# Kernel optimization log

Hardware: AMD Instinct MI355X
Metric: run time of the kernel (lower is better)

The kernel has to match this reference:

```python
import jax, jax.numpy as jnp
import numpy as np

D = 256          # embed_dim
NH = 4           # num_heads
NE = 16          # num_hyperedges
TC = 512         # text_channels
WIN = 64         # window size
EPS = 1e-5


def setup_inputs() -> dict:
    key = jax.random.key(0)
    ks = jax.random.split(key, 20)
    s = 0.02
    return {
        "feature_map": jax.random.normal(ks[0], (8, 256, 64, 64), jnp.float32),
        "text_features": jax.random.normal(ks[1], (8, 64, TC), jnp.float32),
        # qkv_gen: Conv2d(256->256,1x1), GELU, Conv2d(256->768,3x3,pad1), GroupNorm(4,768)
        "conv1_w": jax.random.normal(ks[2], (D, 256, 1, 1), jnp.float32) * s,
        "conv1_b": jnp.zeros((D,), jnp.float32),
        "conv2_w": jax.random.normal(ks[3], (3 * D, D, 3, 3), jnp.float32) * s,
        "conv2_b": jnp.zeros((3 * D,), jnp.float32),
        "gn_w": jnp.ones((3 * D,), jnp.float32),
        "gn_b": jnp.zeros((3 * D,), jnp.float32),
        # shared nn.MultiheadAttention params
        "in_proj_w": jax.random.normal(ks[4], (3 * D, D), jnp.float32) * s,
        "in_proj_b": jnp.zeros((3 * D,), jnp.float32),
        "out_proj_w": jax.random.normal(ks[5], (D, D), jnp.float32) * s,
        "out_proj_b": jnp.zeros((D,), jnp.float32),
        # text_adapter Linear(512->256)
        "txt_w": jax.random.normal(ks[6], (D, TC), jnp.float32) * s,
        "txt_b": jnp.zeros((D,), jnp.float32),
        # edge_predictor: Linear(512->256), GELU, Linear(256->16)
        "ep1_w": jax.random.normal(ks[7], (D, 2 * D), jnp.float32) * s,
        "ep1_b": jnp.zeros((D,), jnp.float32),
        "ep2_w": jax.random.normal(ks[8], (NE, D), jnp.float32) * s,
        "ep2_b": jnp.zeros((NE,), jnp.float32),
    }


def _gelu(x):
    return jax.nn.gelu(x, approximate=False)  # torch default is exact erf GELU


def _conv(x, w, b, pad):
    y = jax.lax.conv_general_dilated(x, w, (1, 1), [(pad, pad), (pad, pad)],
                                     dimension_numbers=("NCHW", "OIHW", "NCHW"))
    return y + b[None, :, None, None]


def _group_norm(x, w, b, groups=4):
    B, C, H, W = x.shape
    xg = x.reshape(B, groups, C // groups, H, W)
    mu = xg.mean(axis=(2, 3, 4), keepdims=True)
    var = xg.var(axis=(2, 3, 4), keepdims=True)
    xg = (xg - mu) * jax.lax.rsqrt(var + EPS)
    return xg.reshape(B, C, H, W) * w[None, :, None, None] + b[None, :, None, None]


def _mha(q, k, v, in_w, in_b, out_w, out_b):
    # torch nn.MultiheadAttention (batch_first), same-dim q/k/v
    Wq, Wk, Wv = in_w[:D], in_w[D:2 * D], in_w[2 * D:]
    bq, bk, bv = in_b[:D], in_b[D:2 * D], in_b[2 * D:]
    dh = D // NH

    def split(x, W, bias):
        y = x @ W.T + bias                      # [B,L,D]
        Bv, L, _ = y.shape
        return y.reshape(Bv, L, NH, dh).transpose(0, 2, 1, 3)  # [B,H,L,dh]

    qh, kh, vh = split(q, Wq, bq), split(k, Wk, bk), split(v, Wv, bv)
    scores = jnp.einsum("bhqd,bhkd->bhqk", qh, kh) / jnp.sqrt(jnp.float32(dh))
    attn = jax.nn.softmax(scores, axis=-1)
    o = jnp.einsum("bhqk,bhkd->bhqd", attn, vh)
    Bv, _, Lq, _ = o.shape
    o = o.transpose(0, 2, 1, 3).reshape(Bv, Lq, D)
    return o @ out_w.T + out_b


def reference(feature_map, text_features, conv1_w, conv1_b, conv2_w, conv2_b,
              gn_w, gn_b, in_proj_w, in_proj_b, out_proj_w, out_proj_b,
              txt_w, txt_b, ep1_w, ep1_b, ep2_w, ep2_b):
    B, C, H, W = feature_map.shape
    N = H * W
    # qkv_gen
    x = _gelu(_conv(feature_map, conv1_w, conv1_b, 0))
    qkv = _group_norm(_conv(x, conv2_w, conv2_b, 1), gn_w, gn_b)
    q, k, v = jnp.split(qkv, 3, axis=1)                    # each [B,D,H,W]
    to_seq = lambda t: t.reshape(B, D, N).transpose(0, 2, 1)  # [B,N,D]
    q_seq, k_seq, v_seq = to_seq(q), to_seq(k), to_seq(v)

    # text_adapter: Linear then AdaptiveAvgPool1d(4) over sequence (L=64 -> 4 bins of 16)
    t = text_features @ txt_w.T + txt_b                    # [B,L,D]
    L = t.shape[1]
    text_feat = t.reshape(B, 4, L // 4, D).mean(axis=2)    # [B,4,D]

    # hierarchical attention
    nw = N // WIN
    q_win = q_seq.reshape(B * nw, WIN, D)
    k_win = k_seq.reshape(B * nw, WIN, D)
    v_win = v_seq.reshape(B * nw, WIN, D)
    local = _mha(q_win, k_win, v_win, in_proj_w, in_proj_b, out_proj_w, out_proj_b)
    local = local.reshape(B, nw, WIN, D)
    global_q = local.mean(axis=2)                          # [B,nw,D]
    glob = _mha(global_q, text_feat, text_feat, in_proj_w, in_proj_b, out_proj_w, out_proj_b)
    glob = jnp.broadcast_to(glob[:, :, None, :], (B, nw, WIN, D))

    combined = jnp.concatenate([local.reshape(B, N, D), glob.reshape(B, N, D)], axis=-1)
    h = _gelu(combined @ ep1_w.T + ep1_b)
    return jax.nn.sigmoid(h @ ep2_w.T + ep2_b)             # [B,N,16]
```

## Files before the change

kernel.cpp:

```cpp
#include <hip/hip_runtime.h>

#define DEV __device__ __forceinline__

typedef __attribute__((ext_vector_type(8))) short bfx8;
typedef __attribute__((ext_vector_type(4))) float fx4;

typedef __attribute__((address_space(3))) unsigned int as3_u32;
typedef const __attribute__((address_space(1))) unsigned int as1_u32c;

DEV void gl_lds16(const void* g, const void* l) {
  __builtin_amdgcn_global_load_lds((as1_u32c*)(unsigned long long)g,
                                   (as3_u32*)(unsigned long long)l, 16, 0, 0);
}

DEV short f2bf(float f) {
  unsigned u = __float_as_uint(f);
  u += 0x7fffu + ((u >> 16) & 1u);
  return (short)(u >> 16);
}
DEV float bf2f(short s) {
  return __uint_as_float(((unsigned)(unsigned short)s) << 16);
}
DEV float gelu_f(float x) { return 0.5f * x * (1.0f + erff(x * 0.70710678118654752f)); }

#define MFMA16(acc, a, b) (acc) = __builtin_amdgcn_mfma_f32_16x16x32_bf16((a), (b), (acc), 0, 0, 0)

struct CvtSeg { const float* src; short* dst; int n; };
struct CvtArgs { CvtSeg s[7]; };

__global__ __launch_bounds__(256) void cvt_multi(CvtArgs a) {
  CvtSeg s = a.s[blockIdx.y];
  int i = ((int)blockIdx.x * 256 + (int)threadIdx.x) * 8;
  if (i >= s.n) return;
  bfx8 o;
  #pragma unroll
  for (int j = 0; j < 8; ++j) o[j] = f2bf(s.src[i + j]);
  *(bfx8*)(s.dst + i) = o;
}

__global__ __launch_bounds__(256) void cvt_conv2w(const float* src, short* dst) {
  int oc = (int)blockIdx.x * 256 + (int)threadIdx.x;
  const float* s = src + (long)oc * 9;
  float t[9];
  #pragma unroll
  for (int j = 0; j < 9; ++j) t[j] = s[j];
  #pragma unroll
  for (int tap = 0; tap < 9; ++tap)
    dst[(long)tap * (768 * 256) + oc] = f2bf(t[tap]);
}

__global__ __launch_bounds__(256) void transpose_wo(const float* ow, short* WoT) {
  __shared__ float tile[64][65];
  int c0 = blockIdx.x * 64, d0 = blockIdx.y * 64;
  int tp = threadIdx.x & 63, tr = threadIdx.x >> 6;
  #pragma unroll
  for (int i = 0; i < 16; ++i) {
    int c = tr + i * 4;
    tile[c][tp] = ow[(long)(c0 + c) * 256 + d0 + tp];
  }
  __syncthreads();
  #pragma unroll
  for (int i = 0; i < 16; ++i) {
    int d = tr + i * 4;
    WoT[(long)(d0 + d) * 256 + c0 + tp] = f2bf(tile[tp][d]);
  }
}

__global__ __launch_bounds__(64) void ebc2(const float* e1w, const float* e1b, const float* ob, float* ebc) {
  int n = blockIdx.x, lane = threadIdx.x;
  float s = 0.0f;
  #pragma unroll
  for (int i = 0; i < 4; ++i) {
    int c = lane + 64 * i;
    s += ob[c] * e1w[(long)n * 512 + c];
  }
  #pragma unroll
  for (int off = 1; off < 64; off <<= 1) s += __shfl_xor(s, off);
  if (lane == 0) ebc[n] = e1b[n] + s;
}

DEV int axc(int p, int c) { return p * 260 + (c ^ (((p >> 2) & 7) << 2)); }

__global__ __launch_bounds__(256) void tc1(const float* fm, const short* W1bf,
                                           const float* b1, short* xP) {
  __shared__ float Af[64 * 260];
  const int lane = threadIdx.x & 63, wv = threadIdx.x >> 6;
  const int lg = lane >> 4, li = lane & 15;
  const int y = blockIdx.x & 63, b = blockIdx.x >> 6;
  const float* src = fm + (long)b * 256 * 4096 + y * 64;
  #pragma unroll
  for (int i = 0; i < 16; ++i) {
    int chunk = i * 256 + (int)threadIdx.x;
    int c = chunk >> 4;
    int q = chunk & 15;
    fx4 v = *(const fx4*)(src + (long)c * 4096 + q * 4);
    #pragma unroll
    for (int j = 0; j < 4; ++j) Af[axc(q * 4 + j, c)] = v[j];
  }
  __syncthreads();

  fx4 acc[4][4] = {};
  const short* Bb = W1bf + (long)(wv * 64 + li) * 256 + lg * 8;
  for (int c0 = 0; c0 < 256; c0 += 32) {
    bfx8 af[4], bfr[4];
    #pragma unroll
    for (int mi = 0; mi < 4; ++mi) {
      int p = mi * 16 + li;
      fx4 lo = *(const fx4*)(&Af[axc(p, c0 + lg * 8)]);
      fx4 hi = *(const fx4*)(&Af[axc(p, c0 + lg * 8 + 4)]);
      bfx8 t;
      t[0] = f2bf(lo[0]); t[1] = f2bf(lo[1]); t[2] = f2bf(lo[2]); t[3] = f2bf(lo[3]);
      t[4] = f2bf(hi[0]); t[5] = f2bf(hi[1]); t[6] = f2bf(hi[2]); t[7] = f2bf(hi[3]);
      af[mi] = t;
    }
    #pragma unroll
    for (int ni = 0; ni < 4; ++ni) bfr[ni] = *(const bfx8*)(Bb + ni * 16 * 256 + c0);
    #pragma unroll
    for (int mi = 0; mi < 4; ++mi)
      #pragma unroll
      for (int ni = 0; ni < 4; ++ni) MFMA16(acc[mi][ni], af[mi], bfr[ni]);
  }

  short* dstP = xP + ((long)b * 66 * 66 + (long)(y + 1) * 66 + 1) * 256;
  #pragma unroll
  for (int mi = 0; mi < 4; ++mi)
    #pragma unroll
    for (int ni = 0; ni < 4; ++ni) {
      int col = wv * 64 + ni * 16 + li;
      float bias = b1[col];
      #pragma unroll
      for (int r = 0; r < 4; ++r) {
        int x = mi * 16 + 4 * lg + r;
        dstP[(long)x * 256 + col] = f2bf(gelu_f(acc[mi][ni][r] + bias));
      }
    }
}

struct GemmP {
  const short* A; const short* B; void* O;
  const float* biasN; const float* biasM; const float* rowbias;
  long lda, ldb, ldo, sA, sB, sO;
  int M, N, K, outF32, act, padHW;
  int aShift;
  long sBN, sBM;
};

__global__ __launch_bounds__(256) void gemm128(GemmP g) {
  __shared__ short As[128 * 32];
  __shared__ short Bs[128 * 32];
  const int lane = threadIdx.x & 63, wv = threadIdx.x >> 6;
  const int wm = wv >> 1, wn = wv & 1;
  const int lg = lane >> 4, li = lane & 15;
  const int m0 = blockIdx.y * 128, n0 = blockIdx.x * 128, z = blockIdx.z;
  const short* A = g.A + (long)z * g.sA + (long)(n0 >> 8) * g.aShift;
  const short* B = g.B + (long)z * g.sB;
  const int srow = wv * 16 + (lane >> 2);
  const int scol = (lane & 3) * 8;
  const short* pA0 = A + (long)(m0 + srow) * g.lda + scol;
  const short* pA1 = A + (long)(m0 + 64 + srow) * g.lda + scol;
  const short* pB0 = B + (long)(n0 + srow) * g.ldb + scol;
  const short* pB1 = B + (long)(n0 + 64 + srow) * g.ldb + scol;
  short* ldsA = As + wv * 512;
  short* ldsB = Bs + wv * 512;
  const short* aRd = As + (wm * 64 + li) * 32 + lg * 8;
  const short* bRd = Bs + (wn * 64 + li) * 32 + lg * 8;

  fx4 acc[4][4] = {};
  for (int kc = 0; kc < g.K; kc += 32) {
    gl_lds16(pA0 + kc, ldsA);
    gl_lds16(pA1 + kc, ldsA + 2048);
    gl_lds16(pB0 + kc, ldsB);
    gl_lds16(pB1 + kc, ldsB + 2048);
    __syncthreads();
    bfx8 af[4], bf[4];
    #pragma unroll
    for (int mi = 0; mi < 4; ++mi) af[mi] = *(const bfx8*)(aRd + mi * 16 * 32);
    #pragma unroll
    for (int ni = 0; ni < 4; ++ni) bf[ni] = *(const bfx8*)(bRd + ni * 16 * 32);
    #pragma unroll
    for (int mi = 0; mi < 4; ++mi)
      #pragma unroll
      for (int ni = 0; ni < 4; ++ni)
        MFMA16(acc[mi][ni], af[mi], bf[ni]);
    __syncthreads();
  }

  #pragma unroll
  for (int mi = 0; mi < 4; ++mi)
    #pragma unroll
    for (int ni = 0; ni < 4; ++ni) {
      int col = n0 + wn * 64 + ni * 16 + li;
      int rowb = m0 + wm * 64 + mi * 16 + 4 * lg;
      float bn = g.biasN ? g.biasN[(long)z * g.sBN + col] : 0.0f;
      #pragma unroll
      for (int r = 0; r < 4; ++r) {
        int row = rowb + r;
        float v = acc[mi][ni][r] + bn;
        if (g.biasM) v += g.biasM[(long)z * g.sBM + row];
        if (g.rowbias) v += g.rowbias[(long)(row >> 6) * g.N + col];
        if (g.act == 1) v = gelu_f(v);
        long orow = row;
        if (g.padHW) orow = (long)((row >> 6) + 1) * 66 + (row & 63) + 1;
        long oidx = (long)z * g.sO + orow * g.ldo + col;
        if (g.outF32) ((float*)g.O)[oidx] = v;
        else ((short*)g.O)[oidx] = f2bf(v);
      }
    }
}

__global__ __launch_bounds__(256) void conv2g(const short* xP, const short* W2t,
                                              const float* b2, short* qkv, float* stats) {
  __shared__ short As[2 * 128 * 32];
  __shared__ short Bs[2 * 128 * 32];
  __shared__ float red[4][4];
  const int lane = threadIdx.x & 63, wv = threadIdx.x >> 6;
  const int wm = wv >> 1, wn = wv & 1;
  const int lg = lane >> 4, li = lane & 15;
  const int w = ((int)blockIdx.x & 7) * 192 + ((int)blockIdx.x >> 3);
  const int n0 = (w % 6) * 128;
  const int by = w / 6;
  const int b = by >> 5, ypair = by & 31;
  const short* xPb = xP + (long)b * 66 * 66 * 256;

  const int srow = wv * 16 + (lane >> 2);
  const int scol = (lane & 3) * 8;
  long baseA[2], baseB[2];
  #pragma unroll
  for (int j = 0; j < 2; ++j) {
    int r = j * 64 + srow;
    int yy = 2 * ypair + (r >> 6);
    int x = r & 63;
    baseA[j] = ((long)yy * 66 + x) * 256 + scol;
    baseB[j] = (long)(n0 + r) * 256 + scol;
  }
  short* ldsA = As + wv * 512;
  short* ldsB = Bs + wv * 512;
  const short* aRd = As + (wm * 64 + li) * 32 + lg * 8;
  const short* bRd = Bs + (wn * 64 + li) * 32 + lg * 8;

  fx4 acc[4][4] = {};
  for (int ks = 0; ks < 36; ++ks) {
    int tap = ks >> 2;
    int c0 = (ks & 3) * 64;
    int dy = tap / 3, dx = tap - dy * 3;
    long aoff = (long)(dy * 66 + dx) * 256 + c0;
    long boff = (long)tap * (768 * 256) + c0;
    gl_lds16(xPb + baseA[0] + aoff, ldsA);
    gl_lds16(xPb + baseA[1] + aoff, ldsA + 2048);
    gl_lds16(xPb + baseA[0] + aoff + 32, ldsA + 4096);
    gl_lds16(xPb + baseA[1] + aoff + 32, ldsA + 6144);
    gl_lds16(W2t + baseB[0] + boff, ldsB);
    gl_lds16(W2t + baseB[1] + boff, ldsB + 2048);
    gl_lds16(W2t + baseB[0] + boff + 32, ldsB + 4096);
    gl_lds16(W2t + baseB[1] + boff + 32, ldsB + 6144);
    __syncthreads();
    #pragma unroll
    for (int kk = 0; kk < 2; ++kk) {
      bfx8 af[4], bf[4];
      #pragma unroll
      for (int mi = 0; mi < 4; ++mi) af[mi] = *(const bfx8*)(aRd + kk * 4096 + mi * 16 * 32);
      #pragma unroll
      for (int ni = 0; ni < 4; ++ni) bf[ni] = *(const bfx8*)(bRd + kk * 4096 + ni * 16 * 32);
      #pragma unroll
      for (int mi = 0; mi < 4; ++mi)
        #pragma unroll
        for (int ni = 0; ni < 4; ++ni)
          MFMA16(acc[mi][ni], af[mi], bf[ni]);
    }
    __syncthreads();
  }

  const int g0 = n0 / 192;
  const int bnd = (g0 + 1) * 192;
  float sA = 0.0f, s2A = 0.0f, sB = 0.0f, s2B = 0.0f;
  const long prow0 = (long)b * 4096 + (long)ypair * 128 + wm * 64 + 4 * lg;
  #pragma unroll
  for (int ni = 0; ni < 4; ++ni) {
    int col = n0 + wn * 64 + ni * 16 + li;
    float bias = b2[col];
    bool inA = (col < bnd);
    #pragma unroll
    for (int mi = 0; mi < 4; ++mi) {
      long rb = prow0 + mi * 16;
      #pragma unroll
      for (int r = 0; r < 4; ++r) {
        float v = acc[mi][ni][r] + bias;
        if (inA) { sA += v; s2A += v * v; } else { sB += v; s2B += v * v; }
        qkv[(rb + r) * 768 + col] = f2bf(v);
      }
    }
  }
  #pragma unroll
  for (int off = 1; off < 64; off <<= 1) {
    sA += __shfl_xor(sA, off);  s2A += __shfl_xor(s2A, off);
    sB += __shfl_xor(sB, off);  s2B += __shfl_xor(s2B, off);
  }
  if (lane == 0) { red[wv][0] = sA; red[wv][1] = s2A; red[wv][2] = sB; red[wv][3] = s2B; }
  __syncthreads();
  if (threadIdx.x == 0) {
    float a1 = red[0][0] + red[1][0] + red[2][0] + red[3][0];
    float a2 = red[0][1] + red[1][1] + red[2][1] + red[3][1];
    atomicAdd(&stats[(b * 4 + g0) * 2], a1);
    atomicAdd(&stats[(b * 4 + g0) * 2 + 1], a2);
    if (bnd < n0 + 128) {
      float b1s = red[0][2] + red[1][2] + red[2][2] + red[3][2];
      float b2s = red[0][3] + red[1][3] + red[2][3] + red[3][3];
      atomicAdd(&stats[(b * 4 + g0 + 1) * 2], b1s);
      atomicAdd(&stats[(b * 4 + g0 + 1) * 2 + 1], b2s);
    }
  }
}

__global__ void gn_fin(const float* stats, float* mufs) {
  int i = threadIdx.x;
  if (i >= 32) return;
  float n = 192.0f * 4096.0f;
  float mu = stats[i * 2] / n;
  float var = stats[i * 2 + 1] / n - mu * mu;
  mufs[i * 2] = mu;
  mufs[i * 2 + 1] = rsqrtf(var + 1e-5f);
}

__global__ __launch_bounds__(256) void gn_fold(const float* mufs, const float* gnw, const float* gnb,
                                               const float* inw, const float* inb,
                                               short* Wf, float* bfold) {
  const int lane = threadIdx.x & 63, wv = threadIdx.x >> 6;
  const int row = blockIdx.x * 4 + wv;
  const int b = row / 768, j = row - b * 768;
  const int cb = (j >> 8) << 8;
  float part = 0.0f;
  #pragma unroll
  for (int i = 0; i < 4; ++i) {
    int c = lane + 64 * i;
    int cg = cb + c;
    int grp = cg / 192;
    float mu = mufs[(b * 4 + grp) * 2];
    float rs = mufs[(b * 4 + grp) * 2 + 1];
    float s = rs * gnw[cg];
    float t = gnb[cg] - mu * s;
    float wv_ = inw[(long)j * 256 + c];
    Wf[(long)row * 256 + c] = f2bf(wv_ * s);
    part += t * wv_;
  }
  #pragma unroll
  for (int off = 1; off < 64; off <<= 1) part += __shfl_xor(part, off);
  if (lane == 0) bfold[row] = inb[j] + part;
}

__global__ __launch_bounds__(256) void attn_local(const short* qk, const short* vhT,
                                                  short* oat, short* oatm) {
  __shared__ short Pl[4 * 64 * 72];
  const int lane = threadIdx.x & 63, h = threadIdx.x >> 6;
  const int lg = lane >> 4, li = lane & 15;
  const int bw = blockIdx.x;
  const int b = bw >> 6, wY = bw & 63;
  const long p0 = (long)bw * 64;

  bfx8 qf[4][2], kf[4][2];
  #pragma unroll
  for (int mi = 0; mi < 4; ++mi)
    #pragma unroll
    for (int ks = 0; ks < 2; ++ks) {
      qf[mi][ks] = *(const bfx8*)(qk + (p0 + 16 * mi + li) * 512 + h * 64 + 32 * ks + 8 * lg);
      kf[mi][ks] = *(const bfx8*)(qk + (p0 + 16 * mi + li) * 512 + 256 + h * 64 + 32 * ks + 8 * lg);
    }
  fx4 s[4][4] = {};
  #pragma unroll
  for (int mi = 0; mi < 4; ++mi)
    #pragma unroll
    for (int ni = 0; ni < 4; ++ni) {
      MFMA16(s[mi][ni], qf[mi][0], kf[ni][0]);
      MFMA16(s[mi][ni], qf[mi][1], kf[ni][1]);
    }
  #pragma unroll
  for (int mi = 0; mi < 4; ++mi)
    #pragma unroll
    for (int ni = 0; ni < 4; ++ni) s[mi][ni] *= 0.125f;

  #pragma unroll
  for (int mi = 0; mi < 4; ++mi)
    #pragma unroll
    for (int r = 0; r < 4; ++r) {
      float mx = fmaxf(fmaxf(s[mi][0][r], s[mi][1][r]), fmaxf(s[mi][2][r], s[mi][3][r]));
      for (int off = 1; off < 16; off <<= 1) mx = fmaxf(mx, __shfl_xor(mx, off));
      float e[4];
      float sum = 0.0f;
      #pragma unroll
      for (int ni = 0; ni < 4; ++ni) { e[ni] = expf(s[mi][ni][r] - mx); sum += e[ni]; }
      for (int off = 1; off < 16; off <<= 1) sum += __shfl_xor(sum, off);
      float inv = 1.0f / sum;
      int row = h * 64 + 16 * mi + 4 * lg + r;
      #pragma unroll
      for (int ni = 0; ni < 4; ++ni) Pl[row * 72 + 16 * ni + li] = f2bf(e[ni] * inv);
    }
  __syncthreads();

  fx4 o[4][4] = {};
  #pragma unroll
  for (int ks = 0; ks < 2; ++ks) {
    bfx8 pf[4], vf[4];
    #pragma unroll
    for (int mi = 0; mi < 4; ++mi)
      pf[mi] = *(const bfx8*)(&Pl[(h * 64 + 16 * mi + li) * 72 + 32 * ks + 8 * lg]);
    #pragma unroll
    for (int ni = 0; ni < 4; ++ni)
      vf[ni] = *(const bfx8*)(vhT + ((long)(b * 256 + h * 64 + 16 * ni + li)) * 4096 + wY * 64 + 32 * ks + 8 * lg);
    #pragma unroll
    for (int mi = 0; mi < 4; ++mi)
      #pragma unroll
      for (int ni = 0; ni < 4; ++ni) MFMA16(o[mi][ni], pf[mi], vf[ni]);
  }
  #pragma unroll
  for (int mi = 0; mi < 4; ++mi)
    #pragma unroll
    for (int ni = 0; ni < 4; ++ni)
      #pragma unroll
      for (int r = 0; r < 4; ++r)
        oat[(p0 + 16 * mi + 4 * lg + r) * 256 + h * 64 + 16 * ni + li] = f2bf(o[mi][ni][r]);

  #pragma unroll
  for (int ni = 0; ni < 4; ++ni) {
    float s2 = 0.0f;
    #pragma unroll
    for (int mi = 0; mi < 4; ++mi)
      #pragma unroll
      for (int r = 0; r < 4; ++r) s2 += o[mi][ni][r];
    s2 += __shfl_xor(s2, 16);
    s2 += __shfl_xor(s2, 32);
    if (lg == 0)
      oatm[(long)bw * 256 + h * 64 + 16 * ni + li] = f2bf(s2 * (1.0f / 64.0f));
  }
}

#define GP 272

DEV void mm_stage(const short* srcA, const short* Bw, long ldb, const float* biasN,
                  short* dstL, float* dstG, int wv, int lg, int li) {
  fx4 acc[4][4] = {};
  const short* aRd = srcA + li * GP + lg * 8;
  const short* bR = Bw + (long)(wv * 64 + li) * ldb + lg * 8;
  for (int kc = 0; kc < 256; kc += 32) {
    bfx8 af[4], bf[4];
    #pragma unroll
    for (int mi = 0; mi < 4; ++mi) af[mi] = *(const bfx8*)(aRd + mi * 16 * GP + kc);
    #pragma unroll
    for (int ni = 0; ni < 4; ++ni) bf[ni] = *(const bfx8*)(bR + (long)ni * 16 * ldb + kc);
    #pragma unroll
    for (int mi = 0; mi < 4; ++mi)
      #pragma unroll
      for (int ni = 0; ni < 4; ++ni) MFMA16(acc[mi][ni], af[mi], bf[ni]);
  }
  #pragma unroll
  for (int mi = 0; mi < 4; ++mi)
    #pragma unroll
    for (int ni = 0; ni < 4; ++ni) {
      int col = wv * 64 + ni * 16 + li;
      float bn = biasN[col];
      #pragma unroll
      for (int r = 0; r < 4; ++r) {
        int row = mi * 16 + 4 * lg + r;
        float v = acc[mi][ni][r] + bn;
        if (dstL) dstL[row * GP + col] = f2bf(v);
        else dstG[(long)row * 256 + col] = v;
      }
    }
}

__global__ __launch_bounds__(256) void globk(
    const short* Tbf, const short* oatm,
    const short* Wtxt, const short* Wqkv, const short* Wo, const short* Wep1,
    const float* tb, const float* ob, const float* inb, const float* ebc,
    float* gcon) {
  __shared__ short bufA[64 * GP];
  __shared__ short bufB[64 * GP];
  __shared__ float tmean_s[4][512];
  __shared__ float tfb_s[4][256];
  __shared__ float kh_s[4][256];
  __shared__ float vh_s[4][256];
  const int t = threadIdx.x;
  const int lane = t & 63, wv = t >> 6;
  const int lg = lane >> 4, li = lane & 15;
  const int b = blockIdx.x;

  {
    int key = t >> 6, d0 = (t & 63) * 8;
    float s[8] = {};
    const short* src = Tbf + ((long)(b * 64 + key * 16)) * 512 + d0;
    for (int i = 0; i < 16; ++i) {
      bfx8 v = *(const bfx8*)(src + i * 512);
      #pragma unroll
      for (int j = 0; j < 8; ++j) s[j] += bf2f(v[j]);
    }
    #pragma unroll
    for (int j = 0; j < 8; ++j) tmean_s[key][d0 + j] = s[j] * (1.0f / 16.0f);
  }
  {
    #pragma unroll
    for (int i = 0; i < 8; ++i) {
      int chunk = i * 256 + t;
      int row = chunk >> 5, colc = (chunk & 31) * 8;
      *(bfx8*)(bufA + row * GP + colc) =
          *(const bfx8*)(oatm + ((long)(b * 64 + row)) * 256 + colc);
    }
  }
  __syncthreads();
  {
    int n = t;
    float a0 = 0, a1 = 0, a2 = 0, a3 = 0;
    const short* wr = Wtxt + (long)n * 512;
    for (int d = 0; d < 512; d += 8) {
      bfx8 w = *(const bfx8*)(wr + d);
      #pragma unroll
      for (int j = 0; j < 8; ++j) {
        float wf = bf2f(w[j]);
        a0 += tmean_s[0][d + j] * wf;
        a1 += tmean_s[1][d + j] * wf;
        a2 += tmean_s[2][d + j] * wf;
        a3 += tmean_s[3][d + j] * wf;
      }
    }
    float bias = tb[n];
    tfb_s[0][n] = a0 + bias; tfb_s[1][n] = a1 + bias;
    tfb_s[2][n] = a2 + bias; tfb_s[3][n] = a3 + bias;
  }
  __syncthreads();
  {
    int n = t;
    const short* wk = Wqkv + (long)(256 + n) * 256;
    const short* wvp = Wqkv + (long)(512 + n) * 256;
    float k0=0,k1=0,k2=0,k3=0,v0=0,v1=0,v2=0,v3=0;
    for (int d = 0; d < 256; d += 8) {
      bfx8 wkv = *(const bfx8*)(wk + d);
      bfx8 wvv = *(const bfx8*)(wvp + d);
      #pragma unroll
      for (int j = 0; j < 8; ++j) {
        float f0 = tfb_s[0][d+j], f1 = tfb_s[1][d+j], f2 = tfb_s[2][d+j], f3 = tfb_s[3][d+j];
        float kw = bf2f(wkv[j]), vw = bf2f(wvv[j]);
        k0 += f0*kw; k1 += f1*kw; k2 += f2*kw; k3 += f3*kw;
        v0 += f0*vw; v1 += f1*vw; v2 += f2*vw; v3 += f3*vw;
      }
    }
    float bk = inb[256+n], bv = inb[512+n];
    kh_s[0][n]=k0+bk; kh_s[1][n]=k1+bk; kh_s[2][n]=k2+bk; kh_s[3][n]=k3+bk;
    vh_s[0][n]=v0+bv; vh_s[1][n]=v1+bv; vh_s[2][n]=v2+bv; vh_s[3][n]=v3+bv;
  }
  mm_stage(bufA, Wo, 256, ob, bufB, nullptr, wv, lg, li);
  __syncthreads();
  mm_stage(bufB, Wqkv, 256, inb, bufA, nullptr, wv, lg, li);
  __syncthreads();
  {
    int p = t >> 2, h = t & 3;
    const short* qr = bufA + p * GP + h * 64;
    float sc[4];
    #pragma unroll
    for (int key = 0; key < 4; ++key) {
      float s = 0.0f;
      for (int d = 0; d < 64; d += 8) {
        bfx8 q8 = *(const bfx8*)(qr + d);
        #pragma unroll
        for (int j = 0; j < 8; ++j) s += bf2f(q8[j]) * kh_s[key][h * 64 + d + j];
      }
      sc[key] = s * 0.125f;
    }
    float mx = fmaxf(fmaxf(sc[0], sc[1]), fmaxf(sc[2], sc[3]));
    float e0 = expf(sc[0]-mx), e1 = expf(sc[1]-mx), e2 = expf(sc[2]-mx), e3 = expf(sc[3]-mx);
    float inv = 1.0f / (e0 + e1 + e2 + e3);
    e0 *= inv; e1 *= inv; e2 *= inv; e3 *= inv;
    short* orow = bufB + p * GP + h * 64;
    for (int d = 0; d < 64; ++d) {
      float o = e0*vh_s[0][h*64+d] + e1*vh_s[1][h*64+d] + e2*vh_s[2][h*64+d] + e3*vh_s[3][h*64+d];
      orow[d] = f2bf(o);
    }
  }
  __syncthreads();
  mm_stage(bufB, Wo, 256, ob, bufA, nullptr, wv, lg, li);
  __syncthreads();
  mm_stage(bufA, Wep1 + 256, 512, ebc, nullptr, gcon + (long)b * 64 * 256, wv, lg, li);
}

__global__ __launch_bounds__(256) void ep2k(const short* hb, const short* w2, const float* b2, float* out) {
  int pp = blockIdx.x * 16 + (threadIdx.x >> 4);
  int e = threadIdx.x & 15;
  const short* hr = hb + (long)pp * 256;
  const short* wr = w2 + (long)e * 256;
  float acc = b2[e];
  for (int k = 0; k < 256; k += 8) {
    bfx8 hv = *(const bfx8*)(hr + k);
    bfx8 wv = *(const bfx8*)(wr + k);
    #pragma unroll
    for (int j = 0; j < 8; ++j) acc += bf2f(hv[j]) * bf2f(wv[j]);
  }
  out[(long)pp * 16 + e] = 1.0f / (1.0f + expf(-acc));
}

extern "C" void kernel_launch(void* const* d_in, const int* in_sizes, int n_in,
                              void* d_out, int out_size, void* d_ws, size_t ws_size,
                              hipStream_t stream) {
  (void)in_sizes; (void)n_in; (void)out_size; (void)ws_size;
  const float* fm  = (const float*)d_in[0];
  const float* txt = (const float*)d_in[1];
  const float* w1  = (const float*)d_in[2];
  const float* b1  = (const float*)d_in[3];
  const float* w2  = (const float*)d_in[4];
  const float* b2  = (const float*)d_in[5];
  const float* gnw = (const float*)d_in[6];
  const float* gnb = (const float*)d_in[7];
  const float* inw = (const float*)d_in[8];
  const float* inb = (const float*)d_in[9];
  const float* ow  = (const float*)d_in[10];
  const float* ob  = (const float*)d_in[11];
  const float* tw  = (const float*)d_in[12];
  const float* tb  = (const float*)d_in[13];
  const float* e1w = (const float*)d_in[14];
  const float* e1b = (const float*)d_in[15];
  const float* e2w = (const float*)d_in[16];
  const float* e2b = (const float*)d_in[17];
  float* out = (float*)d_out;

  char* base = (char*)d_ws;
  size_t off = 0;
  auto alloc = [&](size_t bytes) -> char* {
    char* r = base + off;
    off = (off + bytes + 255) & ~(size_t)255;
    return r;
  };
  short* W1bf = (short*)alloc(256 * 256 * 2);
  short* W2t  = (short*)alloc((size_t)9 * 768 * 256 * 2);
  short* Wqkv = (short*)alloc(768 * 256 * 2);
  short* Wo   = (short*)alloc(256 * 256 * 2);
  short* WoT  = (short*)alloc(256 * 256 * 2);
  short* Wcomb= (short*)alloc(256 * 256 * 2);
  float* ebc  = (float*)alloc(256 * 4);
  short* Wtxt = (short*)alloc(256 * 512 * 2);
  short* Wep1 = (short*)alloc(256 * 512 * 2);
  short* Wep2 = (short*)alloc(16 * 256 * 2);
  short* Tbf  = (short*)alloc((size_t)8 * 64 * 512 * 2);
  short* xP   = (short*)alloc((size_t)8 * 66 * 66 * 256 * 2);
  short* qkv  = (short*)alloc((size_t)8 * 4096 * 768 * 2);
  float* stats= (float*)alloc(64 * 4);
  float* mufs = (float*)alloc(64 * 4);
  short* Wf   = (short*)alloc((size_t)8 * 768 * 256 * 2);
  float* bfold= (float*)alloc((size_t)8 * 768 * 4);
  short* qk   = (short*)alloc((size_t)32768 * 512 * 2);
  short* vhT  = (short*)alloc((size_t)8 * 4096 * 256 * 2);
  short* oat  = (short*)alloc((size_t)8 * 4096 * 256 * 2);
  short* oatm = (short*)alloc(512 * 256 * 2);
  float* gcon = (float*)alloc(512 * 256 * 4);
  short* hbuf = (short*)alloc((size_t)8 * 4096 * 256 * 2);

  hipMemsetAsync(stats, 0, 64 * 4, stream);
  hipMemsetAsync(xP, 0, (size_t)8 * 66 * 66 * 256 * 2, stream);

  CvtArgs ca;
  ca.s[0] = {w1,  W1bf, 256 * 256};
  ca.s[1] = {inw, Wqkv, 768 * 256};
  ca.s[2] = {ow,  Wo,   256 * 256};
  ca.s[3] = {tw,  Wtxt, 256 * 512};
  ca.s[4] = {e1w, Wep1, 256 * 512};
  ca.s[5] = {e2w, Wep2, 16 * 256};
  ca.s[6] = {txt, Tbf,  8 * 64 * 512};
  cvt_multi<<<dim3(128, 7), 256, 0, stream>>>(ca);
  cvt_conv2w<<<768, 256, 0, stream>>>(w2, W2t);
  transpose_wo<<<dim3(4, 4), 256, 0, stream>>>(ow, WoT);
  ebc2<<<256, 64, 0, stream>>>(e1w, e1b, ob, ebc);

  {
    GemmP g{};
    g.A = Wep1; g.lda = 512; g.B = WoT; g.ldb = 256;
    g.O = Wcomb; g.ldo = 256;
    g.M = 256; g.N = 256; g.K = 256;
    gemm128<<<dim3(2, 2, 1), 256, 0, stream>>>(g);
  }

  tc1<<<512, 256, 0, stream>>>(fm, W1bf, b1, xP);

  conv2g<<<1536, 256, 0, stream>>>(xP, W2t, b2, qkv, stats);
  gn_fin<<<1, 32, 0, stream>>>(stats, mufs);
  gn_fold<<<1536, 256, 0, stream>>>(mufs, gnw, gnb, inw, inb, Wf, bfold);

  {
    GemmP g{};
    g.A = qkv; g.lda = 768; g.sA = 4096L * 768;
    g.B = Wf; g.ldb = 256; g.sB = 768L * 256;
    g.O = qk; g.ldo = 512; g.sO = 4096L * 512;
    g.biasN = bfold; g.sBN = 768;
    g.aShift = 256;
    g.M = 4096; g.N = 512; g.K = 256;
    gemm128<<<dim3(4, 32, 8), 256, 0, stream>>>(g);
  }
  {
    GemmP g{};
    g.A = Wf + 512 * 256; g.lda = 256; g.sA = 768L * 256;
    g.B = qkv + 512; g.ldb = 768; g.sB = 4096L * 768;
    g.O = vhT; g.ldo = 4096; g.sO = 256L * 4096;
    g.biasM = bfold + 512; g.sBM = 768;
    g.M = 256; g.N = 4096; g.K = 256;
    gemm128<<<dim3(32, 2, 8), 256, 0, stream>>>(g);
  }

  attn_local<<<512, 256, 0, stream>>>(qk, vhT, oat, oatm);

  globk<<<8, 256, 0, stream>>>(Tbf, oatm, Wtxt, Wqkv, Wo, Wep1,
                               tb, ob, inb, ebc, gcon);

  {
    GemmP g{};
    g.A = oat; g.lda = 256; g.B = Wcomb; g.ldb = 256;
    g.O = hbuf; g.ldo = 256; g.rowbias = gcon; g.act = 1;
    g.M = 32768; g.N = 256; g.K = 256;
    gemm128<<<dim3(2, 256, 1), 256, 0, stream>>>(g);
  }

  ep2k<<<2048, 256, 0, stream>>>(hbuf, Wep2, e2b, out);
}
```

Baseline: 392.0 us.

## Fuse local attention, global attention, edge-predictor GEMM and sigmoid head into one kernel

```diff
diff --git a/kernel.cpp b/kernel.cpp
--- a/kernel.cpp
+++ b/kernel.cpp
@@ -347,141 +347,13 @@
   if (lane == 0) bfold[row] = inb[j] + part;
 }
 
-__global__ __launch_bounds__(256) void attn_local(const short* qk, const short* vhT,
-                                                  short* oat, short* oatm) {
-  __shared__ short Pl[4 * 64 * 72];
-  const int lane = threadIdx.x & 63, h = threadIdx.x >> 6;
-  const int lg = lane >> 4, li = lane & 15;
-  const int bw = blockIdx.x;
-  const int b = bw >> 6, wY = bw & 63;
-  const long p0 = (long)bw * 64;
-
-  bfx8 qf[4][2], kf[4][2];
-  #pragma unroll
-  for (int mi = 0; mi < 4; ++mi)
-    #pragma unroll
-    for (int ks = 0; ks < 2; ++ks) {
-      qf[mi][ks] = *(const bfx8*)(qk + (p0 + 16 * mi + li) * 512 + h * 64 + 32 * ks + 8 * lg);
-      kf[mi][ks] = *(const bfx8*)(qk + (p0 + 16 * mi + li) * 512 + 256 + h * 64 + 32 * ks + 8 * lg);
-    }
-  fx4 s[4][4] = {};
-  #pragma unroll
-  for (int mi = 0; mi < 4; ++mi)
-    #pragma unroll
-    for (int ni = 0; ni < 4; ++ni) {
-      MFMA16(s[mi][ni], qf[mi][0], kf[ni][0]);
-      MFMA16(s[mi][ni], qf[mi][1], kf[ni][1]);
-    }
-  #pragma unroll
-  for (int mi = 0; mi < 4; ++mi)
-    #pragma unroll
-    for (int ni = 0; ni < 4; ++ni) s[mi][ni] *= 0.125f;
-
-  #pragma unroll
-  for (int mi = 0; mi < 4; ++mi)
-    #pragma unroll
-    for (int r = 0; r < 4; ++r) {
-      float mx = fmaxf(fmaxf(s[mi][0][r], s[mi][1][r]), fmaxf(s[mi][2][r], s[mi][3][r]));
-      for (int off = 1; off < 16; off <<= 1) mx = fmaxf(mx, __shfl_xor(mx, off));
-      float e[4];
-      float sum = 0.0f;
-      #pragma unroll
-      for (int ni = 0; ni < 4; ++ni) { e[ni] = expf(s[mi][ni][r] - mx); sum += e[ni]; }
-      for (int off = 1; off < 16; off <<= 1) sum += __shfl_xor(sum, off);
-      float inv = 1.0f / sum;
-      int row = h * 64 + 16 * mi + 4 * lg + r;
-      #pragma unroll
-      for (int ni = 0; ni < 4; ++ni) Pl[row * 72 + 16 * ni + li] = f2bf(e[ni] * inv);
-    }
-  __syncthreads();
-
-  fx4 o[4][4] = {};
-  #pragma unroll
-  for (int ks = 0; ks < 2; ++ks) {
-    bfx8 pf[4], vf[4];
-    #pragma unroll
-    for (int mi = 0; mi < 4; ++mi)
-      pf[mi] = *(const bfx8*)(&Pl[(h * 64 + 16 * mi + li) * 72 + 32 * ks + 8 * lg]);
-    #pragma unroll
-    for (int ni = 0; ni < 4; ++ni)
-      vf[ni] = *(const bfx8*)(vhT + ((long)(b * 256 + h * 64 + 16 * ni + li)) * 4096 + wY * 64 + 32 * ks + 8 * lg);
-    #pragma unroll
-    for (int mi = 0; mi < 4; ++mi)
-      #pragma unroll
-      for (int ni = 0; ni < 4; ++ni) MFMA16(o[mi][ni], pf[mi], vf[ni]);
-  }
-  #pragma unroll
-  for (int mi = 0; mi < 4; ++mi)
-    #pragma unroll
-    for (int ni = 0; ni < 4; ++ni)
-      #pragma unroll
-      for (int r = 0; r < 4; ++r)
-        oat[(p0 + 16 * mi + 4 * lg + r) * 256 + h * 64 + 16 * ni + li] = f2bf(o[mi][ni][r]);
-
-  #pragma unroll
-  for (int ni = 0; ni < 4; ++ni) {
-    float s2 = 0.0f;
-    #pragma unroll
-    for (int mi = 0; mi < 4; ++mi)
-      #pragma unroll
-      for (int r = 0; r < 4; ++r) s2 += o[mi][ni][r];
-    s2 += __shfl_xor(s2, 16);
-    s2 += __shfl_xor(s2, 32);
-    if (lg == 0)
-      oatm[(long)bw * 256 + h * 64 + 16 * ni + li] = f2bf(s2 * (1.0f / 64.0f));
-  }
-}
-
-#define GP 272
-
-DEV void mm_stage(const short* srcA, const short* Bw, long ldb, const float* biasN,
-                  short* dstL, float* dstG, int wv, int lg, int li) {
-  fx4 acc[4][4] = {};
-  const short* aRd = srcA + li * GP + lg * 8;
-  const short* bR = Bw + (long)(wv * 64 + li) * ldb + lg * 8;
-  for (int kc = 0; kc < 256; kc += 32) {
-    bfx8 af[4], bf[4];
-    #pragma unroll
-    for (int mi = 0; mi < 4; ++mi) af[mi] = *(const bfx8*)(aRd + mi * 16 * GP + kc);
-    #pragma unroll
-    for (int ni = 0; ni < 4; ++ni) bf[ni] = *(const bfx8*)(bR + (long)ni * 16 * ldb + kc);
-    #pragma unroll
-    for (int mi = 0; mi < 4; ++mi)
-      #pragma unroll
-      for (int ni = 0; ni < 4; ++ni) MFMA16(acc[mi][ni], af[mi], bf[ni]);
-  }
-  #pragma unroll
-  for (int mi = 0; mi < 4; ++mi)
-    #pragma unroll
-    for (int ni = 0; ni < 4; ++ni) {
-      int col = wv * 64 + ni * 16 + li;
-      float bn = biasN[col];
-      #pragma unroll
-      for (int r = 0; r < 4; ++r) {
-        int row = mi * 16 + 4 * lg + r;
-        float v = acc[mi][ni][r] + bn;
-        if (dstL) dstL[row * GP + col] = f2bf(v);
-        else dstG[(long)row * 256 + col] = v;
-      }
-    }
-}
-
-__global__ __launch_bounds__(256) void globk(
-    const short* Tbf, const short* oatm,
-    const short* Wtxt, const short* Wqkv, const short* Wo, const short* Wep1,
-    const float* tb, const float* ob, const float* inb, const float* ebc,
-    float* gcon) {
-  __shared__ short bufA[64 * GP];
-  __shared__ short bufB[64 * GP];
+__global__ __launch_bounds__(256) void globk_txt(const short* Tbf, const short* Wtxt,
+                                                 const short* Wqkv, const float* tb,
+                                                 const float* inb, float* khv, float* vhv) {
   __shared__ float tmean_s[4][512];
   __shared__ float tfb_s[4][256];
-  __shared__ float kh_s[4][256];
-  __shared__ float vh_s[4][256];
   const int t = threadIdx.x;
-  const int lane = t & 63, wv = t >> 6;
-  const int lg = lane >> 4, li = lane & 15;
   const int b = blockIdx.x;
-
   {
     int key = t >> 6, d0 = (t & 63) * 8;
     float s[8] = {};
@@ -493,15 +365,6 @@
     }
     #pragma unroll
     for (int j = 0; j < 8; ++j) tmean_s[key][d0 + j] = s[j] * (1.0f / 16.0f);
-  }
-  {
-    #pragma unroll
-    for (int i = 0; i < 8; ++i) {
-      int chunk = i * 256 + t;
-      int row = chunk >> 5, colc = (chunk & 31) * 8;
-      *(bfx8*)(bufA + row * GP + colc) =
-          *(const bfx8*)(oatm + ((long)(b * 64 + row)) * 256 + colc);
-    }
   }
   __syncthreads();
   {
@@ -541,56 +404,229 @@
       }
     }
     float bk = inb[256+n], bv = inb[512+n];
-    kh_s[0][n]=k0+bk; kh_s[1][n]=k1+bk; kh_s[2][n]=k2+bk; kh_s[3][n]=k3+bk;
-    vh_s[0][n]=v0+bv; vh_s[1][n]=v1+bv; vh_s[2][n]=v2+bv; vh_s[3][n]=v3+bv;
-  }
-  mm_stage(bufA, Wo, 256, ob, bufB, nullptr, wv, lg, li);
-  __syncthreads();
-  mm_stage(bufB, Wqkv, 256, inb, bufA, nullptr, wv, lg, li);
-  __syncthreads();
-  {
-    int p = t >> 2, h = t & 3;
-    const short* qr = bufA + p * GP + h * 64;
-    float sc[4];
-    #pragma unroll
-    for (int key = 0; key < 4; ++key) {
-      float s = 0.0f;
-      for (int d = 0; d < 64; d += 8) {
-        bfx8 q8 = *(const bfx8*)(qr + d);
-        #pragma unroll
-        for (int j = 0; j < 8; ++j) s += bf2f(q8[j]) * kh_s[key][h * 64 + d + j];
+    khv[(b*4+0)*256+n]=k0+bk; khv[(b*4+1)*256+n]=k1+bk;
+    khv[(b*4+2)*256+n]=k2+bk; khv[(b*4+3)*256+n]=k3+bk;
+    vhv[(b*4+0)*256+n]=v0+bv; vhv[(b*4+1)*256+n]=v1+bv;
+    vhv[(b*4+2)*256+n]=v2+bv; vhv[(b*4+3)*256+n]=v3+bv;
+  }
+}
+
+__global__ __launch_bounds__(256) void attn_mega(
+    const short* qk, const short* vhT, const float* khv, const float* vhv,
+    const short* Wo, const short* Wqkv, const short* Wep1, const short* Wcomb, const short* Wep2,
+    const float* ob, const float* inb, const float* ebc, const float* e2b,
+    float* out) {
+  __shared__ short Pl[4 * 64 * 72];
+  __shared__ float vecA[256], vecB[256], vecG[256];
+  __shared__ float scb[16], pb[16];
+  const int t = threadIdx.x;
+  const int lane = t & 63, h = t >> 6;
+  const int lg = lane >> 4, li = lane & 15;
+  const int bw = blockIdx.x;
+  const int b = bw >> 6, wY = bw & 63;
+  const long p0 = (long)bw * 64;
+
+  bfx8 qf[4][2], kf[4][2];
+  #pragma unroll
+  for (int mi = 0; mi < 4; ++mi)
+    #pragma unroll
+    for (int ks = 0; ks < 2; ++ks) {
+      qf[mi][ks] = *(const bfx8*)(qk + (p0 + 16 * mi + li) * 512 + h * 64 + 32 * ks + 8 * lg);
+      kf[mi][ks] = *(const bfx8*)(qk + (p0 + 16 * mi + li) * 512 + 256 + h * 64 + 32 * ks + 8 * lg);
+    }
+  fx4 s[4][4] = {};
+  #pragma unroll
+  for (int mi = 0; mi < 4; ++mi)
+    #pragma unroll
+    for (int ni = 0; ni < 4; ++ni) {
+      MFMA16(s[mi][ni], qf[mi][0], kf[ni][0]);
+      MFMA16(s[mi][ni], qf[mi][1], kf[ni][1]);
+    }
+  #pragma unroll
+  for (int mi = 0; mi < 4; ++mi)
+    #pragma unroll
+    for (int ni = 0; ni < 4; ++ni) s[mi][ni] *= 0.125f;
+
+  #pragma unroll
+  for (int mi = 0; mi < 4; ++mi)
+    #pragma unroll
+    for (int r = 0; r < 4; ++r) {
+      float mx = fmaxf(fmaxf(s[mi][0][r], s[mi][1][r]), fmaxf(s[mi][2][r], s[mi][3][r]));
+      for (int off = 1; off < 16; off <<= 1) mx = fmaxf(mx, __shfl_xor(mx, off));
+      float e[4];
+      float sum = 0.0f;
+      #pragma unroll
+      for (int ni = 0; ni < 4; ++ni) { e[ni] = expf(s[mi][ni][r] - mx); sum += e[ni]; }
+      for (int off = 1; off < 16; off <<= 1) sum += __shfl_xor(sum, off);
+      float inv = 1.0f / sum;
+      int row = h * 64 + 16 * mi + 4 * lg + r;
+      #pragma unroll
+      for (int ni = 0; ni < 4; ++ni) Pl[row * 72 + 16 * ni + li] = f2bf(e[ni] * inv);
+    }
+  __syncthreads();
+
+  fx4 o[4][4] = {};
+  #pragma unroll
+  for (int ks = 0; ks < 2; ++ks) {
+    bfx8 pf[4], vf[4];
+    #pragma unroll
+    for (int mi = 0; mi < 4; ++mi)
+      pf[mi] = *(const bfx8*)(&Pl[(h * 64 + 16 * mi + li) * 72 + 32 * ks + 8 * lg]);
+    #pragma unroll
+    for (int ni = 0; ni < 4; ++ni)
+      vf[ni] = *(const bfx8*)(vhT + ((long)(b * 256 + h * 64 + 16 * ni + li)) * 4096 + wY * 64 + 32 * ks + 8 * lg);
+    #pragma unroll
+    for (int mi = 0; mi < 4; ++mi)
+      #pragma unroll
+      for (int ni = 0; ni < 4; ++ni) MFMA16(o[mi][ni], pf[mi], vf[ni]);
+  }
+
+  #pragma unroll
+  for (int ni = 0; ni < 4; ++ni) {
+    float s2 = 0.0f;
+    #pragma unroll
+    for (int mi = 0; mi < 4; ++mi)
+      #pragma unroll
+      for (int r = 0; r < 4; ++r) s2 += o[mi][ni][r];
+    s2 += __shfl_xor(s2, 16);
+    s2 += __shfl_xor(s2, 32);
+    if (lg == 0) vecA[h * 64 + 16 * ni + li] = s2 * (1.0f / 64.0f);
+  }
+  __syncthreads();
+
+  short* obuf = Pl;
+  #pragma unroll
+  for (int mi = 0; mi < 4; ++mi)
+    #pragma unroll
+    for (int ni = 0; ni < 4; ++ni)
+      #pragma unroll
+      for (int r = 0; r < 4; ++r)
+        obuf[(16 * mi + 4 * lg + r) * 264 + h * 64 + 16 * ni + li] = f2bf(o[mi][ni][r]);
+
+  {
+    float sum = 0.0f;
+    const short* wr = Wo + (long)t * 256;
+    for (int d = 0; d < 256; d += 8) {
+      bfx8 w8 = *(const bfx8*)(wr + d);
+      #pragma unroll
+      for (int j = 0; j < 8; ++j) sum += vecA[d + j] * bf2f(w8[j]);
+    }
+    vecB[t] = sum + ob[t];
+  }
+  __syncthreads();
+  {
+    float sum = 0.0f;
+    const short* wr = Wqkv + (long)t * 256;
+    for (int d = 0; d < 256; d += 8) {
+      bfx8 w8 = *(const bfx8*)(wr + d);
+      #pragma unroll
+      for (int j = 0; j < 8; ++j) sum += vecB[d + j] * bf2f(w8[j]);
+    }
+    vecG[t] = sum + inb[t];
+  }
+  __syncthreads();
+  if (t < 16) {
+    int key = t & 3, hh = t >> 2;
+    float sum = 0.0f;
+    const float* kr = khv + (long)(b * 4 + key) * 256 + hh * 64;
+    for (int d = 0; d < 64; ++d) sum += vecG[hh * 64 + d] * kr[d];
+    scb[hh * 4 + key] = sum * 0.125f;
+  }
+  __syncthreads();
+  if (t < 4) {
+    float s0 = scb[t*4], s1 = scb[t*4+1], s2 = scb[t*4+2], s3 = scb[t*4+3];
+    float mx = fmaxf(fmaxf(s0, s1), fmaxf(s2, s3));
+    float e0 = expf(s0-mx), e1 = expf(s1-mx), e2 = expf(s2-mx), e3 = expf(s3-mx);
+    float inv = 1.0f / (e0 + e1 + e2 + e3);
+    pb[t*4] = e0*inv; pb[t*4+1] = e1*inv; pb[t*4+2] = e2*inv; pb[t*4+3] = e3*inv;
+  }
+  __syncthreads();
+  {
+    int hh = t >> 6;
+    long base = (long)(b * 4) * 256 + t;
+    vecB[t] = pb[hh*4]   * vhv[base] +
+              pb[hh*4+1] * vhv[base + 256] +
+              pb[hh*4+2] * vhv[base + 512] +
+              pb[hh*4+3] * vhv[base + 768];
+  }
+  __syncthreads();
+  {
+    float sum = 0.0f;
+    const short* wr = Wo + (long)t * 256;
+    for (int d = 0; d < 256; d += 8) {
+      bfx8 w8 = *(const bfx8*)(wr + d);
+      #pragma unroll
+      for (int j = 0; j < 8; ++j) sum += vecB[d + j] * bf2f(w8[j]);
+    }
+    vecA[t] = sum + ob[t];
+  }
+  __syncthreads();
+  {
+    float sum = 0.0f;
+    const short* wr = Wep1 + (long)t * 512 + 256;
+    for (int d = 0; d < 256; d += 8) {
+      bfx8 w8 = *(const bfx8*)(wr + d);
+      #pragma unroll
+      for (int j = 0; j < 8; ++j) sum += vecA[d + j] * bf2f(w8[j]);
+    }
+    vecG[t] = sum + ebc[t];
+  }
+  __syncthreads();
+
+  fx4 hacc[4][4] = {};
+  const short* bR2 = Wcomb + (long)(h * 64 + li) * 256 + lg * 8;
+  for (int kc = 0; kc < 256; kc += 32) {
+    bfx8 af[4], bf[4];
+    #pragma unroll
+    for (int mi = 0; mi < 4; ++mi)
+      af[mi] = *(const bfx8*)(obuf + (mi * 16 + li) * 264 + kc + lg * 8);
+    #pragma unroll
+    for (int ni = 0; ni < 4; ++ni) bf[ni] = *(const bfx8*)(bR2 + (long)ni * 16 * 256 + kc);
+    #pragma unroll
+    for (int mi = 0; mi < 4; ++mi)
+      #pragma unroll
+      for (int ni = 0; ni < 4; ++ni) MFMA16(hacc[mi][ni], af[mi], bf[ni]);
+  }
+  __syncthreads();
+  #pragma unroll
+  for (int mi = 0; mi < 4; ++mi)
+    #pragma unroll
+    for (int ni = 0; ni < 4; ++ni) {
+      int col = h * 64 + ni * 16 + li;
+      #pragma unroll
+      for (int r = 0; r < 4; ++r) {
+        int row = mi * 16 + 4 * lg + r;
+        obuf[row * 264 + col] = f2bf(gelu_f(hacc[mi][ni][r] + vecG[col]));
       }
-      sc[key] = s * 0.125f;
-    }
-    float mx = fmaxf(fmaxf(sc[0], sc[1]), fmaxf(sc[2], sc[3]));
-    float e0 = expf(sc[0]-mx), e1 = expf(sc[1]-mx), e2 = expf(sc[2]-mx), e3 = expf(sc[3]-mx);
-    float inv = 1.0f / (e0 + e1 + e2 + e3);
-    e0 *= inv; e1 *= inv; e2 *= inv; e3 *= inv;
-    short* orow = bufB + p * GP + h * 64;
-    for (int d = 0; d < 64; ++d) {
-      float o = e0*vh_s[0][h*64+d] + e1*vh_s[1][h*64+d] + e2*vh_s[2][h*64+d] + e3*vh_s[3][h*64+d];
-      orow[d] = f2bf(o);
-    }
-  }
-  __syncthreads();
-  mm_stage(bufB, Wo, 256, ob, bufA, nullptr, wv, lg, li);
-  __syncthreads();
-  mm_stage(bufA, Wep1 + 256, 512, ebc, nullptr, gcon + (long)b * 64 * 256, wv, lg, li);
-}
-
-__global__ __launch_bounds__(256) void ep2k(const short* hb, const short* w2, const float* b2, float* out) {
-  int pp = blockIdx.x * 16 + (threadIdx.x >> 4);
-  int e = threadIdx.x & 15;
-  const short* hr = hb + (long)pp * 256;
-  const short* wr = w2 + (long)e * 256;
-  float acc = b2[e];
-  for (int k = 0; k < 256; k += 8) {
-    bfx8 hv = *(const bfx8*)(hr + k);
-    bfx8 wv = *(const bfx8*)(wr + k);
-    #pragma unroll
-    for (int j = 0; j < 8; ++j) acc += bf2f(hv[j]) * bf2f(wv[j]);
-  }
-  out[(long)pp * 16 + e] = 1.0f / (1.0f + expf(-acc));
+    }
+  __syncthreads();
+
+  {
+    int row = t >> 2, eg = (t & 3) * 4;
+    const short* hr = obuf + row * 264;
+    float a0 = e2b[eg], a1 = e2b[eg+1], a2 = e2b[eg+2], a3 = e2b[eg+3];
+    const short* w0 = Wep2 + (long)eg * 256;
+    for (int k = 0; k < 256; k += 8) {
+      bfx8 hv = *(const bfx8*)(hr + k);
+      bfx8 wv0 = *(const bfx8*)(w0 + k);
+      bfx8 wv1 = *(const bfx8*)(w0 + 256 + k);
+      bfx8 wv2 = *(const bfx8*)(w0 + 512 + k);
+      bfx8 wv3 = *(const bfx8*)(w0 + 768 + k);
+      #pragma unroll
+      for (int j = 0; j < 8; ++j) {
+        float hf = bf2f(hv[j]);
+        a0 += hf * bf2f(wv0[j]);
+        a1 += hf * bf2f(wv1[j]);
+        a2 += hf * bf2f(wv2[j]);
+        a3 += hf * bf2f(wv3[j]);
+      }
+    }
+    float* orow = out + (p0 + row) * 16 + eg;
+    orow[0] = 1.0f / (1.0f + expf(-a0));
+    orow[1] = 1.0f / (1.0f + expf(-a1));
+    orow[2] = 1.0f / (1.0f + expf(-a2));
+    orow[3] = 1.0f / (1.0f + expf(-a3));
+  }
 }
 
 extern "C" void kernel_launch(void* const* d_in, const int* in_sizes, int n_in,
@@ -643,10 +679,8 @@
   float* bfold= (float*)alloc((size_t)8 * 768 * 4);
   short* qk   = (short*)alloc((size_t)32768 * 512 * 2);
   short* vhT  = (short*)alloc((size_t)8 * 4096 * 256 * 2);
-  short* oat  = (short*)alloc((size_t)8 * 4096 * 256 * 2);
-  short* oatm = (short*)alloc(512 * 256 * 2);
-  float* gcon = (float*)alloc(512 * 256 * 4);
-  short* hbuf = (short*)alloc((size_t)8 * 4096 * 256 * 2);
+  float* khv  = (float*)alloc(8 * 4 * 256 * 4);
+  float* vhv  = (float*)alloc(8 * 4 * 256 * 4);
 
   hipMemsetAsync(stats, 0, 64 * 4, stream);
   hipMemsetAsync(xP, 0, (size_t)8 * 66 * 66 * 256 * 2, stream);
@@ -663,6 +697,7 @@
   cvt_conv2w<<<768, 256, 0, stream>>>(w2, W2t);
   transpose_wo<<<dim3(4, 4), 256, 0, stream>>>(ow, WoT);
   ebc2<<<256, 64, 0, stream>>>(e1w, e1b, ob, ebc);
+  globk_txt<<<8, 256, 0, stream>>>(Tbf, Wtxt, Wqkv, tb, inb, khv, vhv);
 
   {
     GemmP g{};
@@ -698,18 +733,7 @@
     gemm128<<<dim3(32, 2, 8), 256, 0, stream>>>(g);
   }
 
-  attn_local<<<512, 256, 0, stream>>>(qk, vhT, oat, oatm);
-
-  globk<<<8, 256, 0, stream>>>(Tbf, oatm, Wtxt, Wqkv, Wo, Wep1,
-                               tb, ob, inb, ebc, gcon);
-
-  {
-    GemmP g{};
-    g.A = oat; g.lda = 256; g.B = Wcomb; g.ldb = 256;
-    g.O = hbuf; g.ldo = 256; g.rowbias = gcon; g.act = 1;
-    g.M = 32768; g.N = 256; g.K = 256;
-    gemm128<<<dim3(2, 256, 1), 256, 0, stream>>>(g);
-  }
-
-  ep2k<<<2048, 256, 0, stream>>>(hbuf, Wep2, e2b, out);
-}
+  attn_mega<<<512, 256, 0, stream>>>(qk, vhT, khv, vhv,
+                                     Wo, Wqkv, Wep1, Wcomb, Wep2,
+                                     ob, inb, ebc, e2b, out);
+}
```

After: 382.8 us. -2.3%, faster.
